# Kernel optimization log

Hardware: AMD Instinct MI355X
Metric: run time of the kernel (lower is better)

## Reference

```python
import jax, jax.numpy as jnp
import numpy as np

G = 512          # number of graphs
N = 512          # nodes per graph (equal-sized graphs)
NN = G * N       # total nodes
EG = 8192        # edges per graph (avg degree 16)
C_IN, HID, OUT, K = 128, 32, 2, 20
LATENT = HID * 2 + 1  # 65 = conv1 kernel size & stride


def _gcn(x, W, b, src, dst, deg_inv_sqrt):
    """GCNConv with self-loops: out = D^-1/2 (A+I) D^-1/2 (x W) + b."""
    h = x @ W                                        # [NN, out]
    norm = deg_inv_sqrt[src] * deg_inv_sqrt[dst]     # [E]
    agg = jnp.zeros_like(h).at[dst].add(h[src] * norm[:, None])
    # self-loop message: norm_ii = deg_inv_sqrt[i]^2
    agg = agg + h * (deg_inv_sqrt * deg_inv_sqrt)[:, None]
    return agg + b


def setup_inputs() -> dict:
    key = jax.random.key(0)
    ks = jax.random.split(key, 24)
    x = jax.random.normal(ks[0], (NN, C_IN), jnp.float32)
    offs = (jnp.arange(G, dtype=jnp.int32) * N)[:, None]
    src = (jax.random.randint(ks[1], (G, EG), 0, N, jnp.int32) + offs).reshape(-1)
    dst = (jax.random.randint(ks[2], (G, EG), 0, N, jnp.int32) + offs).reshape(-1)
    edge_index = jnp.stack([src, dst])               # [2, G*EG]
    batch = jnp.repeat(jnp.arange(G, dtype=jnp.int32), N)

    def lin(k, fan_in, shape):
        return jax.random.normal(k, shape, jnp.float32) / np.sqrt(fan_in)

    return {
        "x": x, "edge_index": edge_index, "batch": batch,
        "W0": lin(ks[3], C_IN, (C_IN, HID)), "b0": jnp.zeros((HID,), jnp.float32),
        "W1": lin(ks[4], HID, (HID, HID)),   "b1": jnp.zeros((HID,), jnp.float32),
        "W2": lin(ks[5], HID, (HID, 1)),     "b2": jnp.zeros((1,), jnp.float32),
        "conv1_w": lin(ks[6], LATENT, (16, 1, LATENT)), "conv1_b": jnp.zeros((16,), jnp.float32),
        "conv2_w": lin(ks[7], 16 * 5, (32, 16, 5)),     "conv2_b": jnp.zeros((32,), jnp.float32),
        "lin1_w": lin(ks[8], 192, (192, 128)), "lin1_b": jnp.zeros((128,), jnp.float32),
        "lin2_w": lin(ks[9], 128, (128, OUT)), "lin2_b": jnp.zeros((OUT,), jnp.float32),
    }


def reference(x, edge_index, batch, W0, b0, W1, b1, W2, b2,
              conv1_w, conv1_b, conv2_w, conv2_b,
              lin1_w, lin1_b, lin2_w, lin2_b):
    src, dst = edge_index[0], edge_index[1]
    deg = jnp.zeros((NN,), jnp.float32).at[dst].add(1.0) + 1.0  # +1 self-loop
    dis = jax.lax.rsqrt(deg)

    x1 = jnp.tanh(_gcn(x,  W0, b0, src, dst, dis))   # [NN, 32]
    x2 = jnp.tanh(_gcn(x1, W1, b1, src, dst, dis))   # [NN, 32]
    x3 = jnp.tanh(_gcn(x2, W2, b2, src, dst, dis))   # [NN, 1]
    feat = jnp.concatenate([x1, x2, x3], axis=-1)    # [NN, 65]

    # global_sort_pool: equal-sized contiguous graphs -> reshape, sort by last
    # channel (descending) within each graph, take top-k nodes.
    fg = feat.reshape(G, N, LATENT)
    idx = jnp.argsort(-fg[..., -1], axis=1)[:, :K]                 # [G, K]
    pooled = jnp.take_along_axis(fg, idx[:, :, None], axis=1)      # [G, K, 65]

    # conv1: Conv1d(1,16,kernel=65,stride=65) over flattened [G,1,K*65]
    # == per-sorted-node matmul with the 65-wide kernel.
    h = jax.nn.relu(jnp.einsum('gkc,oc->gok', pooled, conv1_w[:, 0, :])
                    + conv1_b[None, :, None])                      # [G, 16, K]
    h = h.reshape(G, 16, K // 2, 2).max(-1)                        # MaxPool1d(2,2) -> [G,16,10]
    h = jax.nn.relu(
        jax.lax.conv_general_dilated(h, conv2_w, (1,), 'VALID',
                                     dimension_numbers=('NCH', 'OIH', 'NCH'))
        + conv2_b[None, :, None])                                  # [G, 32, 6]
    h = h.reshape(G, -1)                                           # [G, 192]
    h = jax.nn.relu(h @ lin1_w + lin1_b)
    # dropout is identity in eval mode
    return h @ lin2_w + lin2_b                                     # [G, 2]
```

## Files before the change

kernel.cpp:

```cpp
#include <hip/hip_runtime.h>
#include <math.h>

#define G_ 512
#define N_ 512
#define NN_ (G_*N_)
#define EG_ 8192
#define EGP 8704
#define CIN_ 128
#define HID_ 32
#define K_ 20
#define LAT_ 65
#define NSTRIPE 4
#define SW 8
#define HP 513

#define EPS_REL 1.8e-7f

__global__ __launch_bounds__(512) void csr2_kernel(const int* __restrict__ src,
                                                   const int* __restrict__ dst,
                                                   unsigned short* __restrict__ srcl,
                                                   int* __restrict__ gstart,
                                                   unsigned short* __restrict__ nperm,
                                                   double* __restrict__ disd) {
    __shared__ int cnt[N_];
    __shared__ int startv[N_];
    __shared__ int tmpv[N_];
    __shared__ int cursor[N_];
    __shared__ unsigned short binE[EGP];
    int g = blockIdx.x, tid = threadIdx.x;
    const int* ds = dst + (size_t)g * EG_;
    const int* ss = src + (size_t)g * EG_;
    int nb = g * N_;

    cnt[tid] = 0;
    for (int i = tid; i < EGP; i += 512) binE[i] = 0xFFFF;
    __syncthreads();
    for (int e = tid; e < EG_; e += 512) atomicAdd(&cnt[ds[e] - nb], 1);
    __syncthreads();

    {
        int mydeg = cnt[tid];
        int rank = 0;
        for (int j = 0; j < N_; ++j) {
            int dj = cnt[j];
            rank += (dj < mydeg) || (dj == mydeg && j < tid);
        }
        nperm[g * N_ + rank] = (unsigned short)tid;
    }

    int pc = (cnt[tid] + 1) & ~1;
    startv[tid] = pc;
    __syncthreads();
    for (int off = 1; off < N_; off <<= 1) {
        tmpv[tid] = startv[tid] + (tid >= off ? startv[tid - off] : 0);
        __syncthreads();
        startv[tid] = tmpv[tid];
        __syncthreads();
    }

    int excl = startv[tid] - pc;
    cursor[tid] = excl;
    gstart[g * (N_ + 1) + tid] = excl;
    if (tid == 511) gstart[g * (N_ + 1) + N_] = startv[511];
    disd[nb + tid] = 1.0 / sqrt((double)(cnt[tid] + 1));
    __syncthreads();

    for (int e = tid; e < EG_; e += 512) {
        int d = ds[e] - nb;
        int slot = atomicAdd(&cursor[d], 1);
        binE[slot] = (unsigned short)e;
    }
    __syncthreads();

    {
        int n = cnt[tid];
        for (int i = 1; i < n; ++i) {
            unsigned short key = binE[excl + i];
            int j = i - 1;
            while (j >= 0 && binE[excl + j] > key) {
                binE[excl + j + 1] = binE[excl + j];
                --j;
            }
            binE[excl + j + 1] = key;
        }
    }
    __syncthreads();

    for (int i = tid; i < EGP; i += 512) {
        unsigned short e = binE[i];
        srcl[(size_t)g * EGP + i] =
            (e == 0xFFFF) ? (unsigned short)N_ : (unsigned short)(ss[e] - nb);
    }
}

template <int CI>
__global__ __launch_bounds__(256) void mm_kernel(const float* __restrict__ xin,
                                                 const float* __restrict__ W,
                                                 double* __restrict__ h) {
    __shared__ float sx[64][CI + 4];
    __shared__ float sWt[HID_][CI + 4];
    int tid = threadIdx.x;
    for (int i = tid; i < CI * HID_; i += 256) {
        int c = i / HID_, o = i % HID_;
        sWt[o][c] = W[i];
    }
    size_t base = (size_t)blockIdx.x * 64;
    const float4* xsrc = (const float4*)(xin + base * CI);
    for (int i = tid; i < 64 * CI / 4; i += 256) {
        int row = i / (CI / 4), col = (i % (CI / 4)) * 4;
        *(float4*)&sx[row][col] = xsrc[i];
    }
    __syncthreads();

    int o2 = tid & 15, q = tid >> 4;
    int n0 = q * 4;
    double acc[4][2];
#pragma unroll
    for (int j = 0; j < 4; ++j) { acc[j][0] = 0.0; acc[j][1] = 0.0; }

    for (int c = 0; c < CI; c += 4) {
        float4 wa = *(const float4*)&sWt[o2][c];
        float4 wb = *(const float4*)&sWt[o2 + 16][c];
        double w0a = (double)wa.x, w1a = (double)wa.y,
               w2a = (double)wa.z, w3a = (double)wa.w;
        double w0b = (double)wb.x, w1b = (double)wb.y,
               w2b = (double)wb.z, w3b = (double)wb.w;
#pragma unroll
        for (int j = 0; j < 4; ++j) {
            float4 v = *(const float4*)&sx[n0 + j][c];
            double vx = (double)v.x, vy = (double)v.y,
                   vz = (double)v.z, vw = (double)v.w;
            acc[j][0] = fma(vx, w0a, acc[j][0]);
            acc[j][0] = fma(vy, w1a, acc[j][0]);
            acc[j][0] = fma(vz, w2a, acc[j][0]);
            acc[j][0] = fma(vw, w3a, acc[j][0]);
            acc[j][1] = fma(vx, w0b, acc[j][1]);
            acc[j][1] = fma(vy, w1b, acc[j][1]);
            acc[j][1] = fma(vz, w2b, acc[j][1]);
            acc[j][1] = fma(vw, w3b, acc[j][1]);
        }
    }
#pragma unroll
    for (int j = 0; j < 4; ++j) {
#pragma unroll
        for (int p = 0; p < 2; ++p) {
            int o = o2 + 16 * p;
            h[(((size_t)(o >> 3)) * NN_ + base + n0 + j) * SW + (o & 7)] = acc[j][p];
        }
    }
}

__global__ __launch_bounds__(512) void agg_kernel(const double* __restrict__ h,
                                                  const unsigned short* __restrict__ srcl,
                                                  const int* __restrict__ gstart,
                                                  const unsigned short* __restrict__ nperm,
                                                  const double* __restrict__ disd,
                                                  const float* __restrict__ bias,
                                                  float* __restrict__ xoutf) {
    __shared__ double hd2[SW * HP];
    __shared__ unsigned short ssrc[EGP];
    __shared__ unsigned short sstart[N_ + 2];
    __shared__ unsigned short sperm[N_];
    int g = blockIdx.x, st = blockIdx.y, tid = threadIdx.x;
    size_t nbase = (size_t)g * N_;

    for (int i = tid; i < EGP; i += 512) ssrc[i] = srcl[(size_t)g * EGP + i];
    for (int i = tid; i <= N_; i += 512) sstart[i] = (unsigned short)gstart[g * (N_ + 1) + i];
    sperm[tid] = nperm[g * N_ + tid];
    __syncthreads();

    const double* hraw = h + ((size_t)st * NN_ + nbase) * SW;
    const double* dg = disd + nbase;
    for (int i = tid; i < N_ * SW; i += 512) {
        int s = i >> 3, oc = i & 7;
        hd2[oc * HP + s] = hraw[i] * dg[s];
    }
    if (tid < SW) hd2[tid * HP + N_] = -0.0;
    __syncthreads();

    int oc = tid & 7, grp = tid >> 3;
    const double* hrow = hd2 + oc * HP;
    const unsigned int* ssrc32 = (const unsigned int*)ssrc;
    double b = (double)bias[st * SW + oc];

    int nn[8], e0h[8], e1h[8];
    double a[8];
    int mx = 0;
#pragma unroll
    for (int j = 0; j < 8; ++j) {
        int n = sperm[grp * 8 + j];
        nn[j] = n;
        e0h[j] = sstart[n] >> 1;
        e1h[j] = sstart[n + 1] >> 1;
        a[j] = 0.0;
        int d = e1h[j] - e0h[j];
        mx = d > mx ? d : mx;
    }
    for (int t = 0; t < mx; ++t) {
#pragma unroll
        for (int j = 0; j < 8; ++j) {
            int idx = e0h[j] + t;
            if (idx < e1h[j]) {
                unsigned int pr = ssrc32[idx];
                a[j] += hrow[pr & 0xFFFFu];
                a[j] += hrow[pr >> 16];
            }
        }
    }
#pragma unroll
    for (int j = 0; j < 8; ++j) {
        int n = nn[j];
        double dn = dg[n];
        double v = a[j] * dn + hrow[n] * dn + b;
        xoutf[(nbase + n) * HID_ + st * SW + oc] = tanhf((float)v);
    }
}

__global__ __launch_bounds__(512) void gcn3_kernel(const float* __restrict__ xin,
                                                   const float* __restrict__ W2,
                                                   const float* __restrict__ b2,
                                                   const unsigned short* __restrict__ srcl,
                                                   const int* __restrict__ gstart,
                                                   const double* __restrict__ disd,
                                                   float* __restrict__ x3f) {
    __shared__ double h1[N_ + 1];
    __shared__ unsigned short ssrc[EGP];
    __shared__ int sstart[N_ + 1];
    __shared__ double sdis[N_ + 1];
    int g = blockIdx.x, tid = threadIdx.x;
    size_t nbase = (size_t)g * N_;

    for (int i = tid; i < EGP; i += 512) ssrc[i] = srcl[(size_t)g * EGP + i];
    for (int i = tid; i <= N_; i += 512) sstart[i] = gstart[g * (N_ + 1) + i];
    if (tid == 0) { h1[N_] = -0.0; sdis[N_] = 1.0; }
    int n = tid;
    {
        double a = 0.0;
#pragma unroll
        for (int c = 0; c < HID_; ++c)
            a = fma((double)xin[(nbase + n) * HID_ + c], (double)W2[c], a);
        h1[n] = a;
        sdis[n] = disd[nbase + n];
    }
    __syncthreads();

    int e0 = sstart[n], e1 = sstart[n + 1];
    double a = 0.0;
    for (int e = e0; e < e1; ++e) {
        int s = ssrc[e];
        a += h1[s] * sdis[s];
    }
    double dn = sdis[n];
    double v = a * dn + h1[n] * dn * dn + (double)b2[0];
    x3f[nbase + n] = (float)tanh(v);
}

__global__ __launch_bounds__(256) void head_kernel(const float* __restrict__ x1,
                                                   const float* __restrict__ x2,
                                                   const float* __restrict__ x3f,
                                                   const float* __restrict__ c1w,
                                                   const float* __restrict__ c1b,
                                                   const float* __restrict__ c2w,
                                                   const float* __restrict__ c2b,
                                                   const float* __restrict__ l1w,
                                                   const float* __restrict__ l1b,
                                                   const float* __restrict__ l2w,
                                                   const float* __restrict__ l2b,
                                                   float* __restrict__ out) {
    int g = blockIdx.x;
    size_t nbase = (size_t)g * N_;
    __shared__ float sv[N_];
    __shared__ int   topk[K_];
    __shared__ float pooled[K_][LAT_];
    __shared__ float c1[16][K_];
    __shared__ float mp[16][10];
    __shared__ float c2[32 * 6];
    __shared__ float l1[128];

    for (int i = threadIdx.x; i < K_; i += 256) topk[i] = i;
    for (int i = threadIdx.x; i < N_; i += 256) sv[i] = x3f[nbase + i];
    __syncthreads();

    for (int i = threadIdx.x; i < N_; i += 256) {
        float v = sv[i];
        int rank = 0;
        for (int j = 0; j < N_; ++j) {
            float u = sv[j];
            float mag = fmaxf(fabsf(u), fabsf(v));
            bool tie = fabsf(u - v) <= EPS_REL * mag;
            bool beats = tie ? (j < i) : (u > v);
            rank += beats;
        }
        if (rank < K_) topk[rank] = i;
    }
    __syncthreads();

    for (int i = threadIdx.x; i < K_ * LAT_; i += 256) {
        int k = i / LAT_, c = i % LAT_;
        int node = topk[k];
        float f;
        if (c < HID_)            f = x1[(nbase + node) * HID_ + c];
        else if (c < 2 * HID_)   f = x2[(nbase + node) * HID_ + (c - HID_)];
        else                     f = sv[node];
        pooled[k][c] = f;
    }
    __syncthreads();

    for (int i = threadIdx.x; i < 16 * K_; i += 256) {
        int o = i / K_, k = i % K_;
        float acc = c1b[o];
        for (int c = 0; c < LAT_; ++c) acc += pooled[k][c] * c1w[o * LAT_ + c];
        c1[o][k] = fmaxf(acc, 0.f);
    }
    __syncthreads();

    for (int i = threadIdx.x; i < 160; i += 256) {
        int o = i / 10, t = i % 10;
        mp[o][t] = fmaxf(c1[o][2 * t], c1[o][2 * t + 1]);
    }
    __syncthreads();

    for (int i = threadIdx.x; i < 192; i += 256) {
        int o = i / 6, t = i % 6;
        float acc = c2b[o];
        for (int ic = 0; ic < 16; ++ic)
#pragma unroll
            for (int j = 0; j < 5; ++j)
                acc += mp[ic][t + j] * c2w[(o * 16 + ic) * 5 + j];
        c2[o * 6 + t] = fmaxf(acc, 0.f);
    }
    __syncthreads();

    for (int i = threadIdx.x; i < 128; i += 256) {
        float acc = l1b[i];
        for (int c = 0; c < 192; ++c) acc += c2[c] * l1w[c * 128 + i];
        l1[i] = fmaxf(acc, 0.f);
    }
    __syncthreads();

    for (int i = threadIdx.x; i < 2; i += 256) {
        float acc = l2b[i];
        for (int c = 0; c < 128; ++c) acc += l1[c] * l2w[c * 2 + i];
        out[g * 2 + i] = acc;
    }
}

extern "C" void kernel_launch(void* const* d_in, const int* in_sizes, int n_in,
                              void* d_out, int out_size, void* d_ws, size_t ws_size,
                              hipStream_t stream) {
    const float* x   = (const float*)d_in[0];
    const int*   ei  = (const int*)d_in[1];
    const float* W0  = (const float*)d_in[3];
    const float* b0  = (const float*)d_in[4];
    const float* W1  = (const float*)d_in[5];
    const float* b1  = (const float*)d_in[6];
    const float* W2  = (const float*)d_in[7];
    const float* b2  = (const float*)d_in[8];
    const float* c1w = (const float*)d_in[9];
    const float* c1b = (const float*)d_in[10];
    const float* c2w = (const float*)d_in[11];
    const float* c2b = (const float*)d_in[12];
    const float* l1w = (const float*)d_in[13];
    const float* l1b = (const float*)d_in[14];
    const float* l2w = (const float*)d_in[15];
    const float* l2b = (const float*)d_in[16];

    const int* src = ei;
    const int* dst = ei + (size_t)G_ * EG_;

    char* wsb = (char*)d_ws;
    double* h64  = (double*)wsb;                 wsb += (size_t)NN_ * HID_ * 8;
    unsigned short* srcl = (unsigned short*)wsb; wsb += (size_t)G_ * EGP * 2;
    int* gstart = (int*)wsb;                     wsb += (size_t)G_ * (N_ + 1) * 4;
    unsigned short* nperm = (unsigned short*)wsb; wsb += (size_t)G_ * N_ * 2;
    double* disd = (double*)wsb;                 wsb += (size_t)NN_ * 8;
    float*  x3f  = (float*)wsb;                  wsb += (size_t)NN_ * 4;
    float*  x1f  = (float*)wsb;                  wsb += (size_t)NN_ * HID_ * 4;
    float*  x2f  = (float*)wsb;                  wsb += (size_t)NN_ * HID_ * 4;

    dim3 agrid(G_, NSTRIPE);
    csr2_kernel<<<G_, 512, 0, stream>>>(src, dst, srcl, gstart, nperm, disd);
    mm_kernel<CIN_><<<NN_ / 64, 256, 0, stream>>>(x, W0, h64);
    agg_kernel<<<agrid, 512, 0, stream>>>(h64, srcl, gstart, nperm, disd, b0, x1f);
    mm_kernel<HID_><<<NN_ / 64, 256, 0, stream>>>(x1f, W1, h64);
    agg_kernel<<<agrid, 512, 0, stream>>>(h64, srcl, gstart, nperm, disd, b1, x2f);
    gcn3_kernel<<<G_, 512, 0, stream>>>(x2f, W2, b2, srcl, gstart, disd, x3f);
    head_kernel<<<G_, 256, 0, stream>>>(x1f, x2f, x3f, c1w, c1b, c2w, c2b,
                                        l1w, l1b, l2w, l2b, (float*)d_out);
}
```

Measured before the change: 370.7 us.

## Replace quadratic degree ranking with histogram counting sort and vectorize h stores

Node ordering by degree now uses a shared-memory degree histogram with a prefix scan and atomic slot assignment instead of an O(N^2) pairwise rank loop. The matmul kernel remaps output channels so each thread writes two adjacent channels as one double2 store, and pads the weight tile differently. Tie order within equal degrees becomes nondeterministic, degrees of 127 and above share one bucket, and the new padding may misalign the float4 shared loads.

Result: faster. 353.0 us (-4.8%).

```diff
diff --git a/kernel.cpp b/kernel.cpp
--- a/kernel.cpp
+++ b/kernel.cpp
@@ -26,6 +26,7 @@
     __shared__ int startv[N_];
     __shared__ int tmpv[N_];
     __shared__ int cursor[N_];
+    __shared__ int hcur[128];
     __shared__ unsigned short binE[EGP];
     int g = blockIdx.x, tid = threadIdx.x;
     const int* ds = dst + (size_t)g * EG_;
@@ -33,22 +34,27 @@
     int nb = g * N_;
 
     cnt[tid] = 0;
+    if (tid < 128) hcur[tid] = 0;
     for (int i = tid; i < EGP; i += 512) binE[i] = 0xFFFF;
     __syncthreads();
     for (int e = tid; e < EG_; e += 512) atomicAdd(&cnt[ds[e] - nb], 1);
     __syncthreads();
 
+    int mydeg = cnt[tid];
+    int db = mydeg < 127 ? mydeg : 127;
+    atomicAdd(&hcur[db], 1);
+    __syncthreads();
+    if (tid == 0) {
+        int run = 0;
+        for (int d = 0; d < 128; ++d) { int v = hcur[d]; hcur[d] = run; run += v; }
+    }
+    __syncthreads();
     {
-        int mydeg = cnt[tid];
-        int rank = 0;
-        for (int j = 0; j < N_; ++j) {
-            int dj = cnt[j];
-            rank += (dj < mydeg) || (dj == mydeg && j < tid);
-        }
-        nperm[g * N_ + rank] = (unsigned short)tid;
-    }
-
-    int pc = (cnt[tid] + 1) & ~1;
+        int slot = atomicAdd(&hcur[db], 1);
+        nperm[g * N_ + slot] = (unsigned short)tid;
+    }
+
+    int pc = (mydeg + 1) & ~1;
     startv[tid] = pc;
     __syncthreads();
     for (int off = 1; off < N_; off <<= 1) {
@@ -62,7 +68,7 @@
     cursor[tid] = excl;
     gstart[g * (N_ + 1) + tid] = excl;
     if (tid == 511) gstart[g * (N_ + 1) + N_] = startv[511];
-    disd[nb + tid] = 1.0 / sqrt((double)(cnt[tid] + 1));
+    disd[nb + tid] = 1.0 / sqrt((double)(mydeg + 1));
     __syncthreads();
 
     for (int e = tid; e < EG_; e += 512) {
@@ -73,7 +79,7 @@
     __syncthreads();
 
     {
-        int n = cnt[tid];
+        int n = mydeg;
         for (int i = 1; i < n; ++i) {
             unsigned short key = binE[excl + i];
             int j = i - 1;
@@ -98,7 +104,7 @@
                                                  const float* __restrict__ W,
                                                  double* __restrict__ h) {
     __shared__ float sx[64][CI + 4];
-    __shared__ float sWt[HID_][CI + 4];
+    __shared__ float sWt[HID_][CI + 5];
     int tid = threadIdx.x;
     for (int i = tid; i < CI * HID_; i += 256) {
         int c = i / HID_, o = i % HID_;
@@ -119,8 +125,8 @@
     for (int j = 0; j < 4; ++j) { acc[j][0] = 0.0; acc[j][1] = 0.0; }
 
     for (int c = 0; c < CI; c += 4) {
-        float4 wa = *(const float4*)&sWt[o2][c];
-        float4 wb = *(const float4*)&sWt[o2 + 16][c];
+        float4 wa = *(const float4*)&sWt[2 * o2][c];
+        float4 wb = *(const float4*)&sWt[2 * o2 + 1][c];
         double w0a = (double)wa.x, w1a = (double)wa.y,
                w2a = (double)wa.z, w3a = (double)wa.w;
         double w0b = (double)wb.x, w1b = (double)wb.y,
@@ -140,13 +146,14 @@
             acc[j][1] = fma(vw, w3b, acc[j][1]);
         }
     }
+    int stripe = o2 >> 2;
+    int oc = (o2 & 3) * 2;
 #pragma unroll
     for (int j = 0; j < 4; ++j) {
-#pragma unroll
-        for (int p = 0; p < 2; ++p) {
-            int o = o2 + 16 * p;
-            h[(((size_t)(o >> 3)) * NN_ + base + n0 + j) * SW + (o & 7)] = acc[j][p];
-        }
+        double2 val;
+        val.x = acc[j][0];
+        val.y = acc[j][1];
+        *(double2*)&h[(((size_t)stripe) * NN_ + base + n0 + j) * SW + oc] = val;
     }
 }
 
```
